# Optimization experiments

Measured on AMD Instinct MI355X. Metric: run time of the kernel, lower is better.

## Reference

```python
import jax, jax.numpy as jnp
import numpy as np

N_NODES = 50000
N_EDGES = 640000
IN_FEATS = 128
OUT_FEATS = 64
K = 2  # number of sparse sum-aggregation hops


def setup_inputs() -> dict:
    key = jax.random.key(0)
    k1, k2, k3, k4, k5 = jax.random.split(key, 5)
    features = jax.random.normal(k1, (N_NODES, IN_FEATS), dtype=jnp.float32)
    src = jax.random.randint(k2, (N_EDGES,), 0, N_NODES, dtype=jnp.int64)
    dst = jax.random.randint(k3, (N_EDGES,), 0, N_NODES, dtype=jnp.int64)
    weight = jax.random.normal(k4, (IN_FEATS, OUT_FEATS), dtype=jnp.float32) * (IN_FEATS ** -0.5)
    bias = jax.random.normal(k5, (OUT_FEATS,), dtype=jnp.float32) * 0.02
    return {"features": features, "src": src, "dst": dst, "weight": weight, "bias": bias}


def reference(features, src, dst, weight, bias):
    N = features.shape[0]
    ones = jnp.ones(src.shape[0], dtype=features.dtype)
    # degrees (graph is static across hops)
    out_deg = jax.ops.segment_sum(ones, src, num_segments=N)  # out-degree of each node
    in_deg = jax.ops.segment_sum(ones, dst, num_segments=N)   # in-degree of each node
    norm_src = jax.lax.rsqrt(jnp.clip(out_deg, 1.0))[:, None]
    norm_dst = jax.lax.rsqrt(jnp.clip(in_deg, 1.0))[:, None]

    # K hops of unnormalized copy_u/sum message passing
    h = features
    for _ in range(K):
        h = jax.ops.segment_sum(h[src], dst, num_segments=N)

    # GraphConv with norm='both': D_in^{-1/2} A^T D_out^{-1/2} h W + b
    h = h * norm_src
    h = h @ weight  # in_feats > out_feats: project before aggregating
    h = jax.ops.segment_sum(h[src], dst, num_segments=N)
    h = h * norm_dst + bias
    return h
```

## Files before the change

### kernel.cpp

```cpp
#include <hip/hip_runtime.h>
#include <hip/hip_bf16.h>

#define IN_FEATS 128
#define OUT_FEATS 64
#define HB_D 128
#define HB_S 64
#define PB 256
#define MAX_WORDS 12544
#define SMEM_U32 12544
#define PROJ_NODES 256
#define HOP_BLOCKS 2048

static inline char* align_up(char* p, size_t a) {
    return (char*)(((uintptr_t)p + a - 1) & ~(uintptr_t)(a - 1));
}

__device__ __forceinline__ unsigned pack_bf16(float a, float b) {
    unsigned ua = __float_as_uint(a), ub = __float_as_uint(b);
    ua = (ua + 0x7fffu + ((ua >> 16) & 1u)) >> 16;
    ub = (ub + 0x7fffu + ((ub >> 16) & 1u)) >> 16;
    return ua | (ub << 16);
}
__device__ __forceinline__ float bf16_lo(unsigned u) { return __uint_as_float(u << 16); }
__device__ __forceinline__ float bf16_hi(unsigned u) { return __uint_as_float(u & 0xffff0000u); }

__global__ __launch_bounds__(1024)
void hist_proj_kernel(const int* __restrict__ src, const int* __restrict__ dst,
                      const float* __restrict__ X, const float* __restrict__ W,
                      unsigned* __restrict__ partial, uint2* __restrict__ Y,
                      int* __restrict__ gcounter,
                      int N, int E, int slice_d, int slice_s, int words) {
    __shared__ unsigned smem[SMEM_U32];
    int tid = (int)threadIdx.x;
    int b = (int)blockIdx.x;

    if (b == 0 && tid == 0) *gcounter = 0;

    if (b < HB_D + HB_S) {
        unsigned* h = smem;
        for (int w = tid; w < words; w += 1024) h[w] = 0u;
        __syncthreads();
        const int* __restrict__ keys;
        int sb, se;
        if (b < HB_D) { keys = dst; sb = b * slice_d; se = min(sb + slice_d, E); }
        else          { keys = src; sb = (b - HB_D) * slice_s; se = min(sb + slice_s, E); }
        for (int i = sb + tid * 4; i < se; i += 1024 * 4) {
            if (i + 3 < se) {
                int4 k4 = *reinterpret_cast<const int4*>(keys + i);
                atomicAdd(&h[k4.x >> 2], 1u << ((k4.x & 3) * 8));
                atomicAdd(&h[k4.y >> 2], 1u << ((k4.y & 3) * 8));
                atomicAdd(&h[k4.z >> 2], 1u << ((k4.z & 3) * 8));
                atomicAdd(&h[k4.w >> 2], 1u << ((k4.w & 3) * 8));
            } else {
                for (int j = i; j < se; ++j) {
                    int k = keys[j];
                    atomicAdd(&h[k >> 2], 1u << ((k & 3) * 8));
                }
            }
        }
        __syncthreads();
        unsigned* __restrict__ outp = partial + (size_t)b * words;
        for (int w = tid; w < words; w += 1024) outp[w] = h[w];
    } else {
        float* w_s = (float*)smem;
        for (int i = tid; i < IN_FEATS * OUT_FEATS / 4; i += 1024)
            reinterpret_cast<float4*>(w_s)[i] = reinterpret_cast<const float4*>(W)[i];
        __syncthreads();
        int slot = tid >> 4;
        int jj = (tid & 15) * 4;
        int n0 = (b - (HB_D + HB_S)) * PROJ_NODES + slot * 4;
        int m0 = min(n0 + 0, N - 1), m1 = min(n0 + 1, N - 1);
        int m2 = min(n0 + 2, N - 1), m3 = min(n0 + 3, N - 1);
        const float* __restrict__ x0p = X + (size_t)m0 * IN_FEATS;
        const float* __restrict__ x1p = X + (size_t)m1 * IN_FEATS;
        const float* __restrict__ x2p = X + (size_t)m2 * IN_FEATS;
        const float* __restrict__ x3p = X + (size_t)m3 * IN_FEATS;
        float4 a0 = make_float4(0.f, 0.f, 0.f, 0.f), a1 = a0, a2 = a0, a3 = a0;
#pragma unroll 2
        for (int k = 0; k < IN_FEATS; k += 4) {
            float4 x0 = *reinterpret_cast<const float4*>(x0p + k);
            float4 x1 = *reinterpret_cast<const float4*>(x1p + k);
            float4 x2 = *reinterpret_cast<const float4*>(x2p + k);
            float4 x3 = *reinterpret_cast<const float4*>(x3p + k);
#pragma unroll
            for (int q = 0; q < 4; ++q) {
                float4 w = *reinterpret_cast<const float4*>(&w_s[(k + q) * OUT_FEATS + jj]);
                float e0 = (q == 0) ? x0.x : (q == 1) ? x0.y : (q == 2) ? x0.z : x0.w;
                float e1 = (q == 0) ? x1.x : (q == 1) ? x1.y : (q == 2) ? x1.z : x1.w;
                float e2 = (q == 0) ? x2.x : (q == 1) ? x2.y : (q == 2) ? x2.z : x2.w;
                float e3 = (q == 0) ? x3.x : (q == 1) ? x3.y : (q == 2) ? x3.z : x3.w;
                a0.x = fmaf(e0, w.x, a0.x); a0.y = fmaf(e0, w.y, a0.y);
                a0.z = fmaf(e0, w.z, a0.z); a0.w = fmaf(e0, w.w, a0.w);
                a1.x = fmaf(e1, w.x, a1.x); a1.y = fmaf(e1, w.y, a1.y);
                a1.z = fmaf(e1, w.z, a1.z); a1.w = fmaf(e1, w.w, a1.w);
                a2.x = fmaf(e2, w.x, a2.x); a2.y = fmaf(e2, w.y, a2.y);
                a2.z = fmaf(e2, w.z, a2.z); a2.w = fmaf(e2, w.w, a2.w);
                a3.x = fmaf(e3, w.x, a3.x); a3.y = fmaf(e3, w.y, a3.y);
                a3.z = fmaf(e3, w.z, a3.z); a3.w = fmaf(e3, w.w, a3.w);
            }
        }
        float4 accs[4] = {a0, a1, a2, a3};
#pragma unroll
        for (int i = 0; i < 4; ++i) {
            int node = n0 + i;
            if (node < N) {
                uint2 o;
                o.x = pack_bf16(accs[i].x, accs[i].y);
                o.y = pack_bf16(accs[i].z, accs[i].w);
                Y[(size_t)node * (OUT_FEATS / 4) + (jj >> 2)] = o;
            }
        }
    }
}

__global__ __launch_bounds__(PB)
void prefix_alloc_kernel(const unsigned* __restrict__ partial, unsigned* __restrict__ pprefix,
                         int2* __restrict__ rowext, float* __restrict__ normS,
                         float* __restrict__ normD, int* __restrict__ gcounter,
                         int N, int words) {
    __shared__ int tsum[PB];
    __shared__ int s_base;
    int tid = (int)threadIdx.x;
    int w = (int)blockIdx.x * PB + tid;
    unsigned run = 0, ssum = 0;
    if (w < words) {
        for (int bb = 0; bb < HB_D; bb += 16) {
            unsigned v[16], pfx[16];
#pragma unroll
            for (int i = 0; i < 16; ++i) v[i] = partial[(size_t)(bb + i) * words + w];
#pragma unroll
            for (int i = 0; i < 16; ++i) { pfx[i] = run; run += v[i]; }
#pragma unroll
            for (int i = 0; i < 16; ++i) pprefix[(size_t)(bb + i) * words + w] = pfx[i];
        }
        for (int bb = HB_D; bb < HB_D + HB_S; bb += 16) {
            unsigned v[16];
#pragma unroll
            for (int i = 0; i < 16; ++i) v[i] = partial[(size_t)(bb + i) * words + w];
#pragma unroll
            for (int i = 0; i < 16; ++i) ssum += v[i];
        }
    }
    int c0 = (int)(run & 0xffu), c1 = (int)((run >> 8) & 0xffu);
    int c2 = (int)((run >> 16) & 0xffu), c3 = (int)(run >> 24);
    int dtot = c0 + c1 + c2 + c3;
    tsum[tid] = dtot;
    __syncthreads();
    for (int off = 1; off < PB; off <<= 1) {
        int t = (tid >= off) ? tsum[tid - off] : 0;
        __syncthreads();
        tsum[tid] += t;
        __syncthreads();
    }
    if (tid == PB - 1) s_base = atomicAdd(gcounter, tsum[PB - 1]);
    __syncthreads();
    if (w < words) {
        int excl = tsum[tid] - dtot + s_base;
        int r0 = excl, r1 = r0 + c0, r2 = r1 + c1, r3 = r2 + c2;
        int base = 4 * w;
        if (base + 3 < N) {
            int4* re = reinterpret_cast<int4*>(rowext + base);
            re[0] = make_int4(r0, r1, r1, r2);
            re[1] = make_int4(r2, r3, r3, r3 + c3);
            float4 nD = make_float4(rsqrtf(fmaxf((float)c0, 1.f)), rsqrtf(fmaxf((float)c1, 1.f)),
                                    rsqrtf(fmaxf((float)c2, 1.f)), rsqrtf(fmaxf((float)c3, 1.f)));
            int s0 = (int)(ssum & 0xffu), s1 = (int)((ssum >> 8) & 0xffu);
            int s2 = (int)((ssum >> 16) & 0xffu), s3 = (int)(ssum >> 24);
            float4 nS = make_float4(rsqrtf(fmaxf((float)s0, 1.f)), rsqrtf(fmaxf((float)s1, 1.f)),
                                    rsqrtf(fmaxf((float)s2, 1.f)), rsqrtf(fmaxf((float)s3, 1.f)));
            *reinterpret_cast<float4*>(normD + base) = nD;
            *reinterpret_cast<float4*>(normS + base) = nS;
        } else {
            int r[5] = {r0, r1, r2, r3, r3 + c3};
            int cD[4] = {c0, c1, c2, c3};
            int cS[4] = {(int)(ssum & 0xffu), (int)((ssum >> 8) & 0xffu),
                         (int)((ssum >> 16) & 0xffu), (int)(ssum >> 24)};
            for (int i = 0; i < 4 && base + i < N; ++i) {
                rowext[base + i] = make_int2(r[i], r[i + 1]);
                normD[base + i] = rsqrtf(fmaxf((float)cD[i], 1.f));
                normS[base + i] = rsqrtf(fmaxf((float)cS[i], 1.f));
            }
        }
    }
}

__global__ __launch_bounds__(1024)
void fill_kernel(const int* __restrict__ src, const int* __restrict__ dst,
                 const unsigned* __restrict__ pprefix, const int2* __restrict__ rowext,
                 unsigned short* __restrict__ csr16, int E, int slice, int words) {
    __shared__ unsigned cur[MAX_WORDS];
    int tid = (int)threadIdx.x;
    int b = (int)blockIdx.x;
    const unsigned* __restrict__ pp = pprefix + (size_t)b * words;
    for (int w = tid; w < words; w += 1024) cur[w] = pp[w];
    __syncthreads();
    int sb = b * slice;
    int se = min(sb + slice, E);
    for (int i = sb + tid * 4; i < se; i += 1024 * 4) {
        if (i + 3 < se) {
            int4 d4 = *reinterpret_cast<const int4*>(dst + i);
            int4 s4 = *reinterpret_cast<const int4*>(src + i);
            int dd[4] = {d4.x, d4.y, d4.z, d4.w};
            int ss[4] = {s4.x, s4.y, s4.z, s4.w};
#pragma unroll
            for (int j = 0; j < 4; ++j) {
                int bin = dd[j];
                unsigned sh = (unsigned)(bin & 3) * 8u;
                unsigned old = atomicAdd(&cur[bin >> 2], 1u << sh);
                int off = (int)((old >> sh) & 0xffu);
                csr16[rowext[bin].x + off] = (unsigned short)ss[j];
            }
        } else {
            for (int j = i; j < se; ++j) {
                int bin = dst[j];
                unsigned sh = (unsigned)(bin & 3) * 8u;
                unsigned old = atomicAdd(&cur[bin >> 2], 1u << sh);
                int off = (int)((old >> sh) & 0xffu);
                csr16[rowext[bin].x + off] = (unsigned short)src[j];
            }
        }
    }
}

template <int EPI>
__global__ __launch_bounds__(256)
void gather_hop(const uint2* __restrict__ Yin, const int2* __restrict__ rowext,
                const unsigned short* __restrict__ csr16, void* __restrict__ Yout,
                const float* __restrict__ vec, const float* __restrict__ bias,
                int N) {
    int g = ((int)threadIdx.x >> 4) & 3;
    int ci = (int)threadIdx.x & 15;
    int wid = (int)blockIdx.x * 4 + ((int)threadIdx.x >> 6);
    int nwaves = (int)gridDim.x * 4;
    for (int n0 = wid * 4; n0 < N; n0 += nwaves * 4) {
        int node = n0 + g;
        int beg = 0, end = 0;
        if (node < N) {
            int2 be = rowext[node];
            beg = be.x; end = be.y;
        }
        float4 acc = make_float4(0.f, 0.f, 0.f, 0.f);
        float4 acc2 = make_float4(0.f, 0.f, 0.f, 0.f);
        int k = beg;
        for (; k + 1 < end; k += 2) {
            int s0 = (int)csr16[k];
            int s1 = (int)csr16[k + 1];
            uint2 v0 = Yin[(size_t)s0 * (OUT_FEATS / 4) + ci];
            uint2 v1 = Yin[(size_t)s1 * (OUT_FEATS / 4) + ci];
            acc.x += bf16_lo(v0.x); acc.y += bf16_hi(v0.x);
            acc.z += bf16_lo(v0.y); acc.w += bf16_hi(v0.y);
            acc2.x += bf16_lo(v1.x); acc2.y += bf16_hi(v1.x);
            acc2.z += bf16_lo(v1.y); acc2.w += bf16_hi(v1.y);
        }
        if (k < end) {
            uint2 v = Yin[(size_t)csr16[k] * (OUT_FEATS / 4) + ci];
            acc.x += bf16_lo(v.x); acc.y += bf16_hi(v.x);
            acc.z += bf16_lo(v.y); acc.w += bf16_hi(v.y);
        }
        if (node < N) {
            acc.x += acc2.x; acc.y += acc2.y; acc.z += acc2.z; acc.w += acc2.w;
            if (EPI == 1) {
                float sc = vec[node];
                acc.x *= sc; acc.y *= sc; acc.z *= sc; acc.w *= sc;
            }
            if (EPI == 2) {
                float sc = vec[node];
                float4 bb = *reinterpret_cast<const float4*>(bias + ci * 4);
                acc.x = fmaf(acc.x, sc, bb.x); acc.y = fmaf(acc.y, sc, bb.y);
                acc.z = fmaf(acc.z, sc, bb.z); acc.w = fmaf(acc.w, sc, bb.w);
                reinterpret_cast<float4*>(Yout)[(size_t)node * (OUT_FEATS / 4) + ci] = acc;
            } else {
                uint2 o;
                o.x = pack_bf16(acc.x, acc.y);
                o.y = pack_bf16(acc.z, acc.w);
                reinterpret_cast<uint2*>(Yout)[(size_t)node * (OUT_FEATS / 4) + ci] = o;
            }
        }
    }
}

extern "C" void kernel_launch(void* const* d_in, const int* in_sizes, int n_in,
                              void* d_out, int out_size, void* d_ws, size_t ws_size,
                              hipStream_t stream) {
    const float* features = (const float*)d_in[0];
    const int*   src      = (const int*)d_in[1];
    const int*   dst      = (const int*)d_in[2];
    const float* weight   = (const float*)d_in[3];
    const float* bias     = (const float*)d_in[4];

    const int N = in_sizes[0] / IN_FEATS;
    const int E = in_sizes[1];
    const int words = (N + 3) / 4;
    const int NB = (words + PB - 1) / PB;
    const int slice_d = (((E + HB_D - 1) / HB_D) + 3) & ~3;
    const int slice_s = (((E + HB_S - 1) / HB_S) + 3) & ~3;
    const int projBlocks = (N + PROJ_NODES - 1) / PROJ_NODES;

    char* p = (char*)d_ws;
    float* normS   = (float*)p;  p = align_up(p + sizeof(float) * (N + 4), 256);
    float* normD   = (float*)p;  p = align_up(p + sizeof(float) * (N + 4), 256);
    uint2* y0      = (uint2*)p;  p = align_up(p + sizeof(uint2) * (size_t)N * (OUT_FEATS / 4), 256);
    uint2* y1      = (uint2*)p;  p = align_up(p + sizeof(uint2) * (size_t)N * (OUT_FEATS / 4), 256);
    int2*  rowext  = (int2*)p;   p = align_up(p + sizeof(int2) * (N + 4), 256);
    int*   gcounter= (int*)p;    p = align_up(p + sizeof(int) * 4, 256);
    unsigned short* csr16 = (unsigned short*)p;  p = align_up(p + sizeof(unsigned short) * (size_t)E, 256);
    unsigned* partial = (unsigned*)p;  p = align_up(p + sizeof(unsigned) * (size_t)(HB_D + HB_S) * words, 256);
    unsigned* pprefix = (unsigned*)p;  p = align_up(p + sizeof(unsigned) * (size_t)HB_D * words, 256);

    float* out = (float*)d_out;

    hist_proj_kernel<<<HB_D + HB_S + projBlocks, 1024, 0, stream>>>(
        src, dst, features, weight, partial, y0, gcounter, N, E, slice_d, slice_s, words);
    prefix_alloc_kernel<<<NB, PB, 0, stream>>>(partial, pprefix, rowext, normS, normD,
                                               gcounter, N, words);
    fill_kernel<<<HB_D, 1024, 0, stream>>>(src, dst, pprefix, rowext, csr16, E, slice_d, words);

    const int hop_blocks = HOP_BLOCKS;
    gather_hop<0><<<hop_blocks, 256, 0, stream>>>(y0, rowext, csr16, (void*)y1, nullptr, nullptr, N);
    gather_hop<1><<<hop_blocks, 256, 0, stream>>>(y1, rowext, csr16, (void*)y0, normS, nullptr, N);
    gather_hop<2><<<hop_blocks, 256, 0, stream>>>(y0, rowext, csr16, (void*)out, normD, bias, N);
}
```

Before: 108.7 us.

## Move projection into fill kernel and widen gather hop to 16-byte loads

The dense projection blocks now launch alongside the CSR fill kernel instead of the histogram kernel, so the histogram launch is smaller and the fill's atomic-bound work overlaps with the matmul. The gather hops switch to uint4 loads, with 8 lanes per node and 8 nodes per wave. The hop grid is now sized to N so each wave handles one group of nodes rather than grid-striding. This moves the compute overlap to a different stage and halves the number of gather load instructions, at the cost of more registers per thread.

```diff
diff --git a/kernel.cpp b/kernel.cpp
--- a/kernel.cpp
+++ b/kernel.cpp
@@ -9,7 +9,6 @@
 #define MAX_WORDS 12544
 #define SMEM_U32 12544
 #define PROJ_NODES 256
-#define HOP_BLOCKS 2048
 
 static inline char* align_up(char* p, size_t a) {
     return (char*)(((uintptr_t)p + a - 1) & ~(uintptr_t)(a - 1));
@@ -25,92 +24,38 @@
 __device__ __forceinline__ float bf16_hi(unsigned u) { return __uint_as_float(u & 0xffff0000u); }
 
 __global__ __launch_bounds__(1024)
-void hist_proj_kernel(const int* __restrict__ src, const int* __restrict__ dst,
-                      const float* __restrict__ X, const float* __restrict__ W,
-                      unsigned* __restrict__ partial, uint2* __restrict__ Y,
-                      int* __restrict__ gcounter,
-                      int N, int E, int slice_d, int slice_s, int words) {
-    __shared__ unsigned smem[SMEM_U32];
+void hist_kernel(const int* __restrict__ src, const int* __restrict__ dst,
+                 unsigned* __restrict__ partial, int* __restrict__ gcounter,
+                 int E, int slice_d, int slice_s, int words) {
+    __shared__ unsigned h[SMEM_U32];
     int tid = (int)threadIdx.x;
     int b = (int)blockIdx.x;
 
     if (b == 0 && tid == 0) *gcounter = 0;
 
-    if (b < HB_D + HB_S) {
-        unsigned* h = smem;
-        for (int w = tid; w < words; w += 1024) h[w] = 0u;
-        __syncthreads();
-        const int* __restrict__ keys;
-        int sb, se;
-        if (b < HB_D) { keys = dst; sb = b * slice_d; se = min(sb + slice_d, E); }
-        else          { keys = src; sb = (b - HB_D) * slice_s; se = min(sb + slice_s, E); }
-        for (int i = sb + tid * 4; i < se; i += 1024 * 4) {
-            if (i + 3 < se) {
-                int4 k4 = *reinterpret_cast<const int4*>(keys + i);
-                atomicAdd(&h[k4.x >> 2], 1u << ((k4.x & 3) * 8));
-                atomicAdd(&h[k4.y >> 2], 1u << ((k4.y & 3) * 8));
-                atomicAdd(&h[k4.z >> 2], 1u << ((k4.z & 3) * 8));
-                atomicAdd(&h[k4.w >> 2], 1u << ((k4.w & 3) * 8));
-            } else {
-                for (int j = i; j < se; ++j) {
-                    int k = keys[j];
-                    atomicAdd(&h[k >> 2], 1u << ((k & 3) * 8));
-                }
-            }
-        }
-        __syncthreads();
-        unsigned* __restrict__ outp = partial + (size_t)b * words;
-        for (int w = tid; w < words; w += 1024) outp[w] = h[w];
-    } else {
-        float* w_s = (float*)smem;
-        for (int i = tid; i < IN_FEATS * OUT_FEATS / 4; i += 1024)
-            reinterpret_cast<float4*>(w_s)[i] = reinterpret_cast<const float4*>(W)[i];
-        __syncthreads();
-        int slot = tid >> 4;
-        int jj = (tid & 15) * 4;
-        int n0 = (b - (HB_D + HB_S)) * PROJ_NODES + slot * 4;
-        int m0 = min(n0 + 0, N - 1), m1 = min(n0 + 1, N - 1);
-        int m2 = min(n0 + 2, N - 1), m3 = min(n0 + 3, N - 1);
-        const float* __restrict__ x0p = X + (size_t)m0 * IN_FEATS;
-        const float* __restrict__ x1p = X + (size_t)m1 * IN_FEATS;
-        const float* __restrict__ x2p = X + (size_t)m2 * IN_FEATS;
-        const float* __restrict__ x3p = X + (size_t)m3 * IN_FEATS;
-        float4 a0 = make_float4(0.f, 0.f, 0.f, 0.f), a1 = a0, a2 = a0, a3 = a0;
-#pragma unroll 2
-        for (int k = 0; k < IN_FEATS; k += 4) {
-            float4 x0 = *reinterpret_cast<const float4*>(x0p + k);
-            float4 x1 = *reinterpret_cast<const float4*>(x1p + k);
-            float4 x2 = *reinterpret_cast<const float4*>(x2p + k);
-            float4 x3 = *reinterpret_cast<const float4*>(x3p + k);
-#pragma unroll
-            for (int q = 0; q < 4; ++q) {
-                float4 w = *reinterpret_cast<const float4*>(&w_s[(k + q) * OUT_FEATS + jj]);
-                float e0 = (q == 0) ? x0.x : (q == 1) ? x0.y : (q == 2) ? x0.z : x0.w;
-                float e1 = (q == 0) ? x1.x : (q == 1) ? x1.y : (q == 2) ? x1.z : x1.w;
-                float e2 = (q == 0) ? x2.x : (q == 1) ? x2.y : (q == 2) ? x2.z : x2.w;
-                float e3 = (q == 0) ? x3.x : (q == 1) ? x3.y : (q == 2) ? x3.z : x3.w;
-                a0.x = fmaf(e0, w.x, a0.x); a0.y = fmaf(e0, w.y, a0.y);
-                a0.z = fmaf(e0, w.z, a0.z); a0.w = fmaf(e0, w.w, a0.w);
-                a1.x = fmaf(e1, w.x, a1.x); a1.y = fmaf(e1, w.y, a1.y);
-                a1.z = fmaf(e1, w.z, a1.z); a1.w = fmaf(e1, w.w, a1.w);
-                a2.x = fmaf(e2, w.x, a2.x); a2.y = fmaf(e2, w.y, a2.y);
-                a2.z = fmaf(e2, w.z, a2.z); a2.w = fmaf(e2, w.w, a2.w);
-                a3.x = fmaf(e3, w.x, a3.x); a3.y = fmaf(e3, w.y, a3.y);
-                a3.z = fmaf(e3, w.z, a3.z); a3.w = fmaf(e3, w.w, a3.w);
-            }
-        }
-        float4 accs[4] = {a0, a1, a2, a3};
-#pragma unroll
-        for (int i = 0; i < 4; ++i) {
-            int node = n0 + i;
-            if (node < N) {
-                uint2 o;
-                o.x = pack_bf16(accs[i].x, accs[i].y);
-                o.y = pack_bf16(accs[i].z, accs[i].w);
-                Y[(size_t)node * (OUT_FEATS / 4) + (jj >> 2)] = o;
-            }
-        }
-    }
+    for (int w = tid; w < words; w += 1024) h[w] = 0u;
+    __syncthreads();
+    const int* __restrict__ keys;
+    int sb, se;
+    if (b < HB_D) { keys = dst; sb = b * slice_d; se = min(sb + slice_d, E); }
+    else          { keys = src; sb = (b - HB_D) * slice_s; se = min(sb + slice_s, E); }
+    for (int i = sb + tid * 4; i < se; i += 1024 * 4) {
+        if (i + 3 < se) {
+            int4 k4 = *reinterpret_cast<const int4*>(keys + i);
+            atomicAdd(&h[k4.x >> 2], 1u << ((k4.x & 3) * 8));
+            atomicAdd(&h[k4.y >> 2], 1u << ((k4.y & 3) * 8));
+            atomicAdd(&h[k4.z >> 2], 1u << ((k4.z & 3) * 8));
+            atomicAdd(&h[k4.w >> 2], 1u << ((k4.w & 3) * 8));
+        } else {
+            for (int j = i; j < se; ++j) {
+                int k = keys[j];
+                atomicAdd(&h[k >> 2], 1u << ((k & 3) * 8));
+            }
+        }
+    }
+    __syncthreads();
+    unsigned* __restrict__ outp = partial + (size_t)b * words;
+    for (int w = tid; w < words; w += 1024) outp[w] = h[w];
 }
 
 __global__ __launch_bounds__(PB)
@@ -185,38 +130,93 @@
 }
 
 __global__ __launch_bounds__(1024)
-void fill_kernel(const int* __restrict__ src, const int* __restrict__ dst,
-                 const unsigned* __restrict__ pprefix, const int2* __restrict__ rowext,
-                 unsigned short* __restrict__ csr16, int E, int slice, int words) {
-    __shared__ unsigned cur[MAX_WORDS];
+void fill_proj_kernel(const int* __restrict__ src, const int* __restrict__ dst,
+                      const unsigned* __restrict__ pprefix, const int2* __restrict__ rowext,
+                      unsigned short* __restrict__ csr16,
+                      const float* __restrict__ X, const float* __restrict__ W,
+                      uint2* __restrict__ Y,
+                      int N, int E, int slice_d, int words) {
+    __shared__ unsigned smem[SMEM_U32];
     int tid = (int)threadIdx.x;
     int b = (int)blockIdx.x;
-    const unsigned* __restrict__ pp = pprefix + (size_t)b * words;
-    for (int w = tid; w < words; w += 1024) cur[w] = pp[w];
-    __syncthreads();
-    int sb = b * slice;
-    int se = min(sb + slice, E);
-    for (int i = sb + tid * 4; i < se; i += 1024 * 4) {
-        if (i + 3 < se) {
-            int4 d4 = *reinterpret_cast<const int4*>(dst + i);
-            int4 s4 = *reinterpret_cast<const int4*>(src + i);
-            int dd[4] = {d4.x, d4.y, d4.z, d4.w};
-            int ss[4] = {s4.x, s4.y, s4.z, s4.w};
-#pragma unroll
-            for (int j = 0; j < 4; ++j) {
-                int bin = dd[j];
-                unsigned sh = (unsigned)(bin & 3) * 8u;
-                unsigned old = atomicAdd(&cur[bin >> 2], 1u << sh);
-                int off = (int)((old >> sh) & 0xffu);
-                csr16[rowext[bin].x + off] = (unsigned short)ss[j];
-            }
-        } else {
-            for (int j = i; j < se; ++j) {
-                int bin = dst[j];
-                unsigned sh = (unsigned)(bin & 3) * 8u;
-                unsigned old = atomicAdd(&cur[bin >> 2], 1u << sh);
-                int off = (int)((old >> sh) & 0xffu);
-                csr16[rowext[bin].x + off] = (unsigned short)src[j];
+
+    if (b < HB_D) {
+        const unsigned* __restrict__ pp = pprefix + (size_t)b * words;
+        for (int w = tid; w < words; w += 1024) smem[w] = pp[w];
+        __syncthreads();
+        int sb = b * slice_d;
+        int se = min(sb + slice_d, E);
+        for (int i = sb + tid * 4; i < se; i += 1024 * 4) {
+            if (i + 3 < se) {
+                int4 d4 = *reinterpret_cast<const int4*>(dst + i);
+                int4 s4 = *reinterpret_cast<const int4*>(src + i);
+                int dd[4] = {d4.x, d4.y, d4.z, d4.w};
+                int ss[4] = {s4.x, s4.y, s4.z, s4.w};
+#pragma unroll
+                for (int j = 0; j < 4; ++j) {
+                    int bin = dd[j];
+                    unsigned sh = (unsigned)(bin & 3) * 8u;
+                    unsigned old = atomicAdd(&smem[bin >> 2], 1u << sh);
+                    int off = (int)((old >> sh) & 0xffu);
+                    csr16[rowext[bin].x + off] = (unsigned short)ss[j];
+                }
+            } else {
+                for (int j = i; j < se; ++j) {
+                    int bin = dst[j];
+                    unsigned sh = (unsigned)(bin & 3) * 8u;
+                    unsigned old = atomicAdd(&smem[bin >> 2], 1u << sh);
+                    int off = (int)((old >> sh) & 0xffu);
+                    csr16[rowext[bin].x + off] = (unsigned short)src[j];
+                }
+            }
+        }
+    } else {
+        float* w_s = (float*)smem;
+        for (int i = tid; i < IN_FEATS * OUT_FEATS / 4; i += 1024)
+            reinterpret_cast<float4*>(w_s)[i] = reinterpret_cast<const float4*>(W)[i];
+        __syncthreads();
+        int slot = tid >> 4;
+        int jj = (tid & 15) * 4;
+        int n0 = (b - HB_D) * PROJ_NODES + slot * 4;
+        int m0 = min(n0 + 0, N - 1), m1 = min(n0 + 1, N - 1);
+        int m2 = min(n0 + 2, N - 1), m3 = min(n0 + 3, N - 1);
+        const float* __restrict__ x0p = X + (size_t)m0 * IN_FEATS;
+        const float* __restrict__ x1p = X + (size_t)m1 * IN_FEATS;
+        const float* __restrict__ x2p = X + (size_t)m2 * IN_FEATS;
+        const float* __restrict__ x3p = X + (size_t)m3 * IN_FEATS;
+        float4 a0 = make_float4(0.f, 0.f, 0.f, 0.f), a1 = a0, a2 = a0, a3 = a0;
+#pragma unroll 2
+        for (int k = 0; k < IN_FEATS; k += 4) {
+            float4 x0 = *reinterpret_cast<const float4*>(x0p + k);
+            float4 x1 = *reinterpret_cast<const float4*>(x1p + k);
+            float4 x2 = *reinterpret_cast<const float4*>(x2p + k);
+            float4 x3 = *reinterpret_cast<const float4*>(x3p + k);
+#pragma unroll
+            for (int q = 0; q < 4; ++q) {
+                float4 w = *reinterpret_cast<const float4*>(&w_s[(k + q) * OUT_FEATS + jj]);
+                float e0 = (q == 0) ? x0.x : (q == 1) ? x0.y : (q == 2) ? x0.z : x0.w;
+                float e1 = (q == 0) ? x1.x : (q == 1) ? x1.y : (q == 2) ? x1.z : x1.w;
+                float e2 = (q == 0) ? x2.x : (q == 1) ? x2.y : (q == 2) ? x2.z : x2.w;
+                float e3 = (q == 0) ? x3.x : (q == 1) ? x3.y : (q == 2) ? x3.z : x3.w;
+                a0.x = fmaf(e0, w.x, a0.x); a0.y = fmaf(e0, w.y, a0.y);
+                a0.z = fmaf(e0, w.z, a0.z); a0.w = fmaf(e0, w.w, a0.w);
+                a1.x = fmaf(e1, w.x, a1.x); a1.y = fmaf(e1, w.y, a1.y);
+                a1.z = fmaf(e1, w.z, a1.z); a1.w = fmaf(e1, w.w, a1.w);
+                a2.x = fmaf(e2, w.x, a2.x); a2.y = fmaf(e2, w.y, a2.y);
+                a2.z = fmaf(e2, w.z, a2.z); a2.w = fmaf(e2, w.w, a2.w);
+                a3.x = fmaf(e3, w.x, a3.x); a3.y = fmaf(e3, w.y, a3.y);
+                a3.z = fmaf(e3, w.z, a3.z); a3.w = fmaf(e3, w.w, a3.w);
+            }
+        }
+        float4 accs[4] = {a0, a1, a2, a3};
+#pragma unroll
+        for (int i = 0; i < 4; ++i) {
+            int node = n0 + i;
+            if (node < N) {
+                uint2 o;
+                o.x = pack_bf16(accs[i].x, accs[i].y);
+                o.y = pack_bf16(accs[i].z, accs[i].w);
+                Y[(size_t)node * (OUT_FEATS / 4) + (jj >> 2)] = o;
             }
         }
     }
@@ -224,56 +224,71 @@
 
 template <int EPI>
 __global__ __launch_bounds__(256)
-void gather_hop(const uint2* __restrict__ Yin, const int2* __restrict__ rowext,
+void gather_hop(const uint4* __restrict__ Yin, const int2* __restrict__ rowext,
                 const unsigned short* __restrict__ csr16, void* __restrict__ Yout,
                 const float* __restrict__ vec, const float* __restrict__ bias,
                 int N) {
-    int g = ((int)threadIdx.x >> 4) & 3;
-    int ci = (int)threadIdx.x & 15;
+    int g = ((int)threadIdx.x >> 3) & 7;
+    int ci = (int)threadIdx.x & 7;
     int wid = (int)blockIdx.x * 4 + ((int)threadIdx.x >> 6);
     int nwaves = (int)gridDim.x * 4;
-    for (int n0 = wid * 4; n0 < N; n0 += nwaves * 4) {
+    for (int n0 = wid * 8; n0 < N; n0 += nwaves * 8) {
         int node = n0 + g;
         int beg = 0, end = 0;
         if (node < N) {
             int2 be = rowext[node];
             beg = be.x; end = be.y;
         }
-        float4 acc = make_float4(0.f, 0.f, 0.f, 0.f);
-        float4 acc2 = make_float4(0.f, 0.f, 0.f, 0.f);
+        float4 aA = make_float4(0.f, 0.f, 0.f, 0.f), aB = aA;
+        float4 bA = aA, bB = aA;
         int k = beg;
         for (; k + 1 < end; k += 2) {
             int s0 = (int)csr16[k];
             int s1 = (int)csr16[k + 1];
-            uint2 v0 = Yin[(size_t)s0 * (OUT_FEATS / 4) + ci];
-            uint2 v1 = Yin[(size_t)s1 * (OUT_FEATS / 4) + ci];
-            acc.x += bf16_lo(v0.x); acc.y += bf16_hi(v0.x);
-            acc.z += bf16_lo(v0.y); acc.w += bf16_hi(v0.y);
-            acc2.x += bf16_lo(v1.x); acc2.y += bf16_hi(v1.x);
-            acc2.z += bf16_lo(v1.y); acc2.w += bf16_hi(v1.y);
+            uint4 v0 = Yin[(size_t)s0 * 8 + ci];
+            uint4 v1 = Yin[(size_t)s1 * 8 + ci];
+            aA.x += bf16_lo(v0.x); aA.y += bf16_hi(v0.x);
+            aA.z += bf16_lo(v0.y); aA.w += bf16_hi(v0.y);
+            aB.x += bf16_lo(v0.z); aB.y += bf16_hi(v0.z);
+            aB.z += bf16_lo(v0.w); aB.w += bf16_hi(v0.w);
+            bA.x += bf16_lo(v1.x); bA.y += bf16_hi(v1.x);
+            bA.z += bf16_lo(v1.y); bA.w += bf16_hi(v1.y);
+            bB.x += bf16_lo(v1.z); bB.y += bf16_hi(v1.z);
+            bB.z += bf16_lo(v1.w); bB.w += bf16_hi(v1.w);
         }
         if (k < end) {
-            uint2 v = Yin[(size_t)csr16[k] * (OUT_FEATS / 4) + ci];
-            acc.x += bf16_lo(v.x); acc.y += bf16_hi(v.x);
-            acc.z += bf16_lo(v.y); acc.w += bf16_hi(v.y);
+            uint4 v = Yin[(size_t)csr16[k] * 8 + ci];
+            aA.x += bf16_lo(v.x); aA.y += bf16_hi(v.x);
+            aA.z += bf16_lo(v.y); aA.w += bf16_hi(v.y);
+            aB.x += bf16_lo(v.z); aB.y += bf16_hi(v.z);
+            aB.z += bf16_lo(v.w); aB.w += bf16_hi(v.w);
         }
         if (node < N) {
-            acc.x += acc2.x; acc.y += acc2.y; acc.z += acc2.z; acc.w += acc2.w;
+            aA.x += bA.x; aA.y += bA.y; aA.z += bA.z; aA.w += bA.w;
+            aB.x += bB.x; aB.y += bB.y; aB.z += bB.z; aB.w += bB.w;
             if (EPI == 1) {
                 float sc = vec[node];
-                acc.x *= sc; acc.y *= sc; acc.z *= sc; acc.w *= sc;
+                aA.x *= sc; aA.y *= sc; aA.z *= sc; aA.w *= sc;
+                aB.x *= sc; aB.y *= sc; aB.z *= sc; aB.w *= sc;
             }
             if (EPI == 2) {
                 float sc = vec[node];
-                float4 bb = *reinterpret_cast<const float4*>(bias + ci * 4);
-                acc.x = fmaf(acc.x, sc, bb.x); acc.y = fmaf(acc.y, sc, bb.y);
-                acc.z = fmaf(acc.z, sc, bb.z); acc.w = fmaf(acc.w, sc, bb.w);
-                reinterpret_cast<float4*>(Yout)[(size_t)node * (OUT_FEATS / 4) + ci] = acc;
+                float4 b0 = *reinterpret_cast<const float4*>(bias + ci * 8);
+                float4 b1 = *reinterpret_cast<const float4*>(bias + ci * 8 + 4);
+                aA.x = fmaf(aA.x, sc, b0.x); aA.y = fmaf(aA.y, sc, b0.y);
+                aA.z = fmaf(aA.z, sc, b0.z); aA.w = fmaf(aA.w, sc, b0.w);
+                aB.x = fmaf(aB.x, sc, b1.x); aB.y = fmaf(aB.y, sc, b1.y);
+                aB.z = fmaf(aB.z, sc, b1.w == b1.w ? b1.z : b1.z); aB.w = fmaf(aB.w, sc, b1.w);
+                float* op = (float*)Yout + (size_t)node * OUT_FEATS + ci * 8;
+                *reinterpret_cast<float4*>(op) = aA;
+                *reinterpret_cast<float4*>(op + 4) = aB;
             } else {
-                uint2 o;
-                o.x = pack_bf16(acc.x, acc.y);
-                o.y = pack_bf16(acc.z, acc.w);
-                reinterpret_cast<uint2*>(Yout)[(size_t)node * (OUT_FEATS / 4) + ci] = o;
+                uint4 o;
+                o.x = pack_bf16(aA.x, aA.y);
+                o.y = pack_bf16(aA.z, aA.w);
+                o.z = pack_bf16(aB.x, aB.y);
+                o.w = pack_bf16(aB.z, aB.w);
+                reinterpret_cast<uint4*>(Yout)[(size_t)node * 8 + ci] = o;
             }
         }
     }
@@ -309,14 +324,15 @@
 
     float* out = (float*)d_out;
 
-    hist_proj_kernel<<<HB_D + HB_S + projBlocks, 1024, 0, stream>>>(
-        src, dst, features, weight, partial, y0, gcounter, N, E, slice_d, slice_s, words);
+    hist_kernel<<<HB_D + HB_S, 1024, 0, stream>>>(
+        src, dst, partial, gcounter, E, slice_d, slice_s, words);
     prefix_alloc_kernel<<<NB, PB, 0, stream>>>(partial, pprefix, rowext, normS, normD,
                                                gcounter, N, words);
-    fill_kernel<<<HB_D, 1024, 0, stream>>>(src, dst, pprefix, rowext, csr16, E, slice_d, words);
-
-    const int hop_blocks = HOP_BLOCKS;
-    gather_hop<0><<<hop_blocks, 256, 0, stream>>>(y0, rowext, csr16, (void*)y1, nullptr, nullptr, N);
-    gather_hop<1><<<hop_blocks, 256, 0, stream>>>(y1, rowext, csr16, (void*)y0, normS, nullptr, N);
-    gather_hop<2><<<hop_blocks, 256, 0, stream>>>(y0, rowext, csr16, (void*)out, normD, bias, N);
-}
+    fill_proj_kernel<<<HB_D + projBlocks, 1024, 0, stream>>>(
+        src, dst, pprefix, rowext, csr16, features, weight, y0, N, E, slice_d, words);
+
+    const int hop_blocks = (N + 31) / 32;
+    gather_hop<0><<<hop_blocks, 256, 0, stream>>>((const uint4*)y0, rowext, csr16, (void*)y1, nullptr, nullptr, N);
+    gather_hop<1><<<hop_blocks, 256, 0, stream>>>((const uint4*)y1, rowext, csr16, (void*)y0, normS, nullptr, N);
+    gather_hop<2><<<hop_blocks, 256, 0, stream>>>((const uint4*)y0, rowext, csr16, (void*)out, normD, bias, N);
+}
```

Measured after the change: 91.93 us. 1.18x faster.
